# Optimization experiments

Measured on AMD Instinct MI355X. Metric: run time of the kernel, lower is better.

Reference implementation:

```python
import jax, jax.numpy as jnp
import numpy as np
import math

B, T, D, H = 4, 2048, 1024, 16
DH = D // H

def setup_inputs() -> dict:
    key = jax.random.key(0)
    ks = jax.random.split(key, 12)
    s = 1.0 / math.sqrt(D)
    inp = {
        'q': jax.random.normal(ks[0], (B, T, D), jnp.float32),
        'k': jax.random.normal(ks[1], (B, T, D), jnp.float32),
        'v': jax.random.normal(ks[2], (B, T, D), jnp.float32),
        # causal attn_mask [B, Tq, Tk]; all-keep padding mask [B,1,1,Tk]
        'attn_mask': jnp.broadcast_to(jnp.tril(jnp.ones((T, T), jnp.bool_)), (B, T, T)),
        'key_keep_mask': jnp.ones((B, 1, 1, T), jnp.bool_),
        'wq_w': jax.random.normal(ks[3], (D, D), jnp.float32) * s,
        'wq_b': jnp.zeros((D,), jnp.float32),
        'wk_w': jax.random.normal(ks[4], (D, D), jnp.float32) * s,
        'wk_b': jnp.zeros((D,), jnp.float32),
        'wv_w': jax.random.normal(ks[5], (D, D), jnp.float32) * s,
        'wv_b': jnp.zeros((D,), jnp.float32),
        'wo_w': jax.random.normal(ks[6], (D, D), jnp.float32) * s,
        'wo_b': jnp.zeros((D,), jnp.float32),
    }
    return inp

def reference(q, k, v, attn_mask, key_keep_mask, wq_w, wq_b, wk_w, wk_b, wv_w, wv_b, wo_w, wo_b):
    # projections (torch Linear: x @ W^T + b)
    Q = (q @ wq_w.T + wq_b).reshape(B, -1, H, DH).transpose(0, 2, 1, 3)  # [B,H,Tq,DH]
    K = (k @ wk_w.T + wk_b).reshape(B, -1, H, DH).transpose(0, 2, 1, 3)
    V = (v @ wv_w.T + wv_b).reshape(B, -1, H, DH).transpose(0, 2, 1, 3)
    scores = jnp.einsum('bhqd,bhkd->bhqk', Q, K) / math.sqrt(DH)
    neg_inf = jnp.array(-jnp.inf, scores.dtype)
    scores = jnp.where(attn_mask[:, None, :, :], scores, neg_inf)
    scores = jnp.where(key_keep_mask, scores, neg_inf)
    attn = jax.nn.softmax(scores, axis=-1)  # dropout p=0 -> identity
    out = jnp.einsum('bhqk,bhkd->bhqd', attn, V)
    out = out.transpose(0, 2, 1, 3).reshape(B, -1, D)
    return out @ wo_w.T + wo_b
```

## Files before the change

### kernel.cpp

```cpp
#include <hip/hip_runtime.h>
#include <cstdint>
#include <cstddef>


typedef float f32x4 __attribute__((ext_vector_type(4)));
typedef short bf16x8 __attribute__((ext_vector_type(8)));
typedef float fltx4 __attribute__((ext_vector_type(4)));
typedef unsigned short u16x4 __attribute__((ext_vector_type(4)));

#define GLOBAL_AS __attribute__((address_space(1)))
#define LDS_AS __attribute__((address_space(3)))

__device__ __forceinline__ unsigned short f2bf(float f) {
    union { float f; unsigned int u; } x;
    x.f = f;
    unsigned int u = x.u;
    unsigned int r = (u + 0x7FFFu + ((u >> 16) & 1u)) >> 16;
    return (unsigned short)r;
}

__device__ __forceinline__ unsigned int pack_trunc(float a, float b) {
    union { float f; unsigned int u; } x, y;
    x.f = a; y.f = b;
    return (x.u >> 16) | (y.u & 0xFFFF0000u);
}

__global__ __launch_bounds__(256) void cast_all_kernel(
    const float* __restrict__ q, const float* __restrict__ k, const float* __restrict__ v,
    const float* __restrict__ wq, const float* __restrict__ wk,
    const float* __restrict__ wv, const float* __restrict__ wo,
    unsigned short* __restrict__ dst)
{
    const size_t SEG = 8388608;
    const size_t WSEG = 1048576;
    size_t i = ((size_t)blockIdx.x * 256 + threadIdx.x) * 4;
    const float* src;
    size_t off;
    if (i < SEG)               { src = q;  off = i; }
    else if (i < 2 * SEG)      { src = k;  off = i - SEG; }
    else if (i < 3 * SEG)      { src = v;  off = i - 2 * SEG; }
    else if (i < 3 * SEG + WSEG)     { src = wq; off = i - 3 * SEG; }
    else if (i < 3 * SEG + 2 * WSEG) { src = wk; off = i - 3 * SEG - WSEG; }
    else if (i < 3 * SEG + 3 * WSEG) { src = wv; off = i - 3 * SEG - 2 * WSEG; }
    else                             { src = wo; off = i - 3 * SEG - 3 * WSEG; }
    fltx4 val = *(const fltx4*)(src + off);
    u16x4 o;
    o[0] = f2bf(val[0]);
    o[1] = f2bf(val[1]);
    o[2] = f2bf(val[2]);
    o[3] = f2bf(val[3]);
    *(u16x4*)(dst + i) = o;
}

__global__ __launch_bounds__(512, 2) void qkv_gemm_kernel(
    const unsigned short* __restrict__ X,
    const unsigned short* __restrict__ Wc,
    const float* __restrict__ bq, const float* __restrict__ bk,
    const float* __restrict__ bv,
    unsigned short* __restrict__ Outs,
    float qscale)
{
    const int z = blockIdx.y;
    const unsigned short* A  = X  + (size_t)z * 8388608;
    const unsigned short* Bw = Wc + (size_t)z * 1048576;
    const float* bias = (z == 0) ? bq : (z == 1) ? bk : bv;
    unsigned short* outp = Outs + (size_t)z * 8388608;
    const float scale = (z == 0) ? qscale : 1.0f;
    const bool vmode = (z == 2);

    __shared__ __align__(16) unsigned short lds[3 * 24576];

    const int tid = threadIdx.x;
    const int w = tid >> 6, lane = tid & 63;
    const int quad = lane >> 4, l16 = lane & 15;
    const int wr = w >> 1, wc = w & 1;

    const int lin = blockIdx.x;
    const int r_ = lin & 7, s_ = lin >> 3;
    const int bm = (r_ * 4 + (s_ & 3)) * 256;
    const int bn = (s_ >> 2) * 128;

    const int rsub = lane >> 3;
    const int csw = (lane & 7) ^ rsub;

    auto stage_half = [&](int kt, int buf, int half) {
        unsigned short* lA = lds + buf * 24576;
        unsigned short* lB = lA + 16384;
        const unsigned short* Ab = A + (size_t)bm * 1024 + kt * 64;
        const unsigned short* Bb = Bw + (size_t)bn * 1024 + kt * 64;
#pragma unroll
        for (int j = 0; j < 2; ++j) {
            int r0 = w * 32 + (half * 2 + j) * 8;
            __builtin_amdgcn_global_load_lds(
                (const GLOBAL_AS unsigned int*)(Ab + (size_t)(r0 + rsub) * 1024 + csw * 8),
                (LDS_AS unsigned int*)(lA + r0 * 64), 16, 0, 0);
        }
        {
            int r0 = w * 16 + half * 8;
            __builtin_amdgcn_global_load_lds(
                (const GLOBAL_AS unsigned int*)(Bb + (size_t)(r0 + rsub) * 1024 + csw * 8),
                (LDS_AS unsigned int*)(lB + r0 * 64), 16, 0, 0);
        }
    };

    f32x4 acc[4][4] = {};

    stage_half(0, 0, 0); stage_half(0, 0, 1);
    stage_half(1, 1, 0); stage_half(1, 1, 1);
    asm volatile("s_waitcnt vmcnt(6)" ::: "memory");
    __builtin_amdgcn_s_barrier();

    for (int kt = 0; kt < 16; ++kt) {
        const int cur = kt % 3;
        const int nxt = (kt + 2) % 3;
        const bool pre = (kt < 14);
        const unsigned short* lA = lds + cur * 24576;
        const unsigned short* lB = lA + 16384;

#pragma unroll
        for (int kh = 0; kh < 2; ++kh) {
            bf16x8 af[4], bfr[4];
#pragma unroll
            for (int mi = 0; mi < 4; ++mi) {
                int row = wr * 64 + mi * 16 + l16;
                af[mi] = *(const bf16x8*)(lA + (size_t)row * 64 +
                                          (((kh * 4 + quad) ^ (row & 7)) * 8));
            }
#pragma unroll
            for (int ni = 0; ni < 4; ++ni) {
                int row = wc * 64 + ni * 16 + l16;
                bfr[ni] = *(const bf16x8*)(lB + (size_t)row * 64 +
                                           (((kh * 4 + quad) ^ (row & 7)) * 8));
            }
            if (pre) stage_half(kt + 2, nxt, kh);

            __builtin_amdgcn_s_barrier();
            asm volatile("s_waitcnt lgkmcnt(0)" ::: "memory");
            __builtin_amdgcn_sched_barrier(0);
            __builtin_amdgcn_s_setprio(1);
#pragma unroll
            for (int mi = 0; mi < 4; ++mi)
#pragma unroll
                for (int ni = 0; ni < 4; ++ni)
                    acc[mi][ni] = __builtin_amdgcn_mfma_f32_16x16x32_bf16(
                        af[mi], bfr[ni], acc[mi][ni], 0, 0, 0);
            __builtin_amdgcn_s_setprio(0);
            __builtin_amdgcn_sched_barrier(0);

            if (kh == 0) {
                __builtin_amdgcn_s_barrier();
            } else {
                if (kt < 14)       asm volatile("s_waitcnt vmcnt(6)" ::: "memory");
                else if (kt == 14) asm volatile("s_waitcnt vmcnt(0)" ::: "memory");
                if (kt < 15) __builtin_amdgcn_s_barrier();
            }
        }
    }

#pragma unroll
    for (int mi = 0; mi < 4; ++mi) {
        int rowb = bm + wr * 64 + mi * 16 + quad * 4;
#pragma unroll
        for (int ni = 0; ni < 4; ++ni) {
            int col = bn + wc * 64 + ni * 16 + l16;
            float bv_ = bias[col];
#pragma unroll
            for (int r = 0; r < 4; ++r) {
                int m = rowb + r;
                float vout = (acc[mi][ni][r] + bv_) * scale;
                int b = m >> 11, t = m & 2047, h = col >> 6, d = col & 63;
                if (!vmode) {
                    outp[((size_t)(b * 16 + h) * 2048 + t) * 64 + d] = f2bf(vout);
                } else {
                    outp[((size_t)(b * 16 + h) * 64 + d) * 2048 + t] = f2bf(vout);
                }
            }
        }
    }
}

__global__ __launch_bounds__(512, 2) void out_gemm_kernel(
    const unsigned short* __restrict__ A,
    const unsigned short* __restrict__ Bw,
    const float* __restrict__ bias,
    float* __restrict__ outp)
{
    __shared__ __align__(16) unsigned short lds[3 * 24576];

    const int tid = threadIdx.x;
    const int w = tid >> 6, lane = tid & 63;
    const int quad = lane >> 4, l16 = lane & 15;
    const int wr = w >> 1, wc = w & 1;

    const int lin = blockIdx.x;
    const int r_ = lin & 7, s_ = lin >> 3;
    const int bm = (r_ * 4 + (s_ & 3)) * 256;
    const int bn = (s_ >> 2) * 128;

    const int rsub = lane >> 3;
    const int csw = (lane & 7) ^ rsub;

    auto stage_half = [&](int kt, int buf, int half) {
        unsigned short* lA = lds + buf * 24576;
        unsigned short* lB = lA + 16384;
        const unsigned short* Ab = A + (size_t)bm * 1024 + kt * 64;
        const unsigned short* Bb = Bw + (size_t)bn * 1024 + kt * 64;
#pragma unroll
        for (int j = 0; j < 2; ++j) {
            int r0 = w * 32 + (half * 2 + j) * 8;
            __builtin_amdgcn_global_load_lds(
                (const GLOBAL_AS unsigned int*)(Ab + (size_t)(r0 + rsub) * 1024 + csw * 8),
                (LDS_AS unsigned int*)(lA + r0 * 64), 16, 0, 0);
        }
        {
            int r0 = w * 16 + half * 8;
            __builtin_amdgcn_global_load_lds(
                (const GLOBAL_AS unsigned int*)(Bb + (size_t)(r0 + rsub) * 1024 + csw * 8),
                (LDS_AS unsigned int*)(lB + r0 * 64), 16, 0, 0);
        }
    };

    f32x4 acc[4][4] = {};

    stage_half(0, 0, 0); stage_half(0, 0, 1);
    stage_half(1, 1, 0); stage_half(1, 1, 1);
    asm volatile("s_waitcnt vmcnt(6)" ::: "memory");
    __builtin_amdgcn_s_barrier();

    for (int kt = 0; kt < 16; ++kt) {
        const int cur = kt % 3;
        const int nxt = (kt + 2) % 3;
        const bool pre = (kt < 14);
        const unsigned short* lA = lds + cur * 24576;
        const unsigned short* lB = lA + 16384;

#pragma unroll
        for (int kh = 0; kh < 2; ++kh) {
            bf16x8 af[4], bfr[4];
#pragma unroll
            for (int mi = 0; mi < 4; ++mi) {
                int row = wr * 64 + mi * 16 + l16;
                af[mi] = *(const bf16x8*)(lA + (size_t)row * 64 +
                                          (((kh * 4 + quad) ^ (row & 7)) * 8));
            }
#pragma unroll
            for (int ni = 0; ni < 4; ++ni) {
                int row = wc * 64 + ni * 16 + l16;
                bfr[ni] = *(const bf16x8*)(lB + (size_t)row * 64 +
                                           (((kh * 4 + quad) ^ (row & 7)) * 8));
            }
            if (pre) stage_half(kt + 2, nxt, kh);

            __builtin_amdgcn_s_barrier();
            asm volatile("s_waitcnt lgkmcnt(0)" ::: "memory");
            __builtin_amdgcn_sched_barrier(0);
            __builtin_amdgcn_s_setprio(1);
#pragma unroll
            for (int mi = 0; mi < 4; ++mi)
#pragma unroll
                for (int ni = 0; ni < 4; ++ni)
                    acc[mi][ni] = __builtin_amdgcn_mfma_f32_16x16x32_bf16(
                        af[mi], bfr[ni], acc[mi][ni], 0, 0, 0);
            __builtin_amdgcn_s_setprio(0);
            __builtin_amdgcn_sched_barrier(0);

            if (kh == 0) {
                __builtin_amdgcn_s_barrier();
            } else {
                if (kt < 14)       asm volatile("s_waitcnt vmcnt(6)" ::: "memory");
                else if (kt == 14) asm volatile("s_waitcnt vmcnt(0)" ::: "memory");
                if (kt < 15) __builtin_amdgcn_s_barrier();
            }
        }
    }

#pragma unroll
    for (int mi = 0; mi < 4; ++mi) {
        int rowb = bm + wr * 64 + mi * 16 + quad * 4;
#pragma unroll
        for (int ni = 0; ni < 4; ++ni) {
            int col = bn + wc * 64 + ni * 16 + l16;
            float bv_ = bias[col];
#pragma unroll
            for (int r = 0; r < 4; ++r)
                outp[(size_t)(rowb + r) * 1024 + col] = acc[mi][ni][r] + bv_;
        }
    }
}

__global__ __launch_bounds__(256) void attn_kernel(
    const unsigned short* __restrict__ Qh,
    const unsigned short* __restrict__ Kh,
    const unsigned short* __restrict__ Vt,
    unsigned short* __restrict__ att)
{
    const int tid = threadIdx.x;
    const int w = tid >> 6, lane = tid & 63;
    const int qd = lane >> 4, l16 = lane & 15;
    const int bh = blockIdx.x;
    const int pairy = blockIdx.y;

    const unsigned short* Qp = Qh + (size_t)bh * 2048 * 64;
    const unsigned short* Kp = Kh + (size_t)bh * 2048 * 64;
    const unsigned short* Vp = Vt + (size_t)bh * 64 * 2048;
    const int b = bh >> 4, h = bh & 15;

    __shared__ __align__(16) unsigned short Kl[3][64 * 64];
    __shared__ __align__(16) unsigned short Vl[3][64 * 64];
    __shared__ __align__(16) unsigned short Pl[4][2][16 * 64];

    auto stage = [&](int kt, int buf) {
#pragma unroll
        for (int j = 0; j < 2; ++j) {
            int r = w * 16 + j * 8 + (lane >> 3);
            int c = (lane & 7) ^ (r & 7);
            __builtin_amdgcn_global_load_lds(
                (const GLOBAL_AS unsigned int*)(Kp + (size_t)(kt * 64 + r) * 64 + c * 8),
                (LDS_AS unsigned int*)(&Kl[buf][(w * 16 + j * 8) * 64]), 16, 0, 0);
            __builtin_amdgcn_global_load_lds(
                (const GLOBAL_AS unsigned int*)(Vp + (size_t)r * 2048 + kt * 64 + c * 8),
                (LDS_AS unsigned int*)(&Vl[buf][(w * 16 + j * 8) * 64]), 16, 0, 0);
        }
    };

    auto run_phase = [&](int qblk) {
        const int wqbase = qblk * 128 + w * 32;
        const int ktmax = 2 * qblk + 1;

        bf16x8 qa[2][2];
#pragma unroll
        for (int qt = 0; qt < 2; ++qt)
#pragma unroll
            for (int ks = 0; ks < 2; ++ks)
                qa[qt][ks] = *(const bf16x8*)(Qp + (size_t)(wqbase + qt * 16 + l16) * 64 + ks * 32 + qd * 8);

        float lp[2] = {0.0f, 0.0f};
        f32x4 O[2][4] = {};

        __builtin_amdgcn_s_barrier();
        stage(0, 0);
        stage(1, 1);

        for (int kt = 0; kt <= ktmax; ++kt) {
            if (kt < ktmax) asm volatile("s_waitcnt vmcnt(4)" ::: "memory");
            else            asm volatile("s_waitcnt vmcnt(0)" ::: "memory");
            __builtin_amdgcn_s_barrier();
            if (kt + 2 <= ktmax) stage(kt + 2, (kt + 2) % 3);

            if (kt * 64 <= wqbase + 31) {
                const unsigned short* kl = &Kl[kt % 3][0];
                const unsigned short* vl = &Vl[kt % 3][0];

                bf16x8 kf[4][2];
#pragma unroll
                for (int nt = 0; nt < 4; ++nt)
#pragma unroll
                    for (int ks = 0; ks < 2; ++ks)
                        kf[nt][ks] = *(const bf16x8*)(kl + (nt * 16 + l16) * 64 +
                                                      (((ks * 4 + qd) ^ (l16 & 7)) * 8));

                f32x4 S[2][4];
                __builtin_amdgcn_s_setprio(1);
#pragma unroll
                for (int qt = 0; qt < 2; ++qt)
#pragma unroll
                    for (int nt = 0; nt < 4; ++nt) {
                        f32x4 a = {};
                        a = __builtin_amdgcn_mfma_f32_16x16x32_bf16(kf[nt][0], qa[qt][0], a, 0, 0, 0);
                        a = __builtin_amdgcn_mfma_f32_16x16x32_bf16(kf[nt][1], qa[qt][1], a, 0, 0, 0);
                        S[qt][nt] = a;
                    }
                __builtin_amdgcn_s_setprio(0);

                bf16x8 vf[2][4];
#pragma unroll
                for (int s = 0; s < 2; ++s)
#pragma unroll
                    for (int dh = 0; dh < 4; ++dh)
                        vf[s][dh] = *(const bf16x8*)(vl + (dh * 16 + l16) * 64 +
                                                     (((s * 4 + qd) ^ (l16 & 7)) * 8));

                if (kt * 64 + 63 > wqbase) {
#pragma unroll
                    for (int qt = 0; qt < 2; ++qt) {
                        int qrow = wqbase + qt * 16 + l16;
#pragma unroll
                        for (int nt = 0; nt < 4; ++nt) {
                            int kbase = kt * 64 + nt * 16 + qd * 4;
#pragma unroll
                            for (int r = 0; r < 4; ++r)
                                if (kbase + r > qrow) S[qt][nt][r] = -INFINITY;
                        }
                    }
                }

#pragma unroll
                for (int qt = 0; qt < 2; ++qt) {
                    float s0 = 0.0f;
#pragma unroll
                    for (int nt = 0; nt < 4; ++nt)
#pragma unroll
                        for (int r = 0; r < 4; ++r) {
                            float e = __builtin_amdgcn_exp2f(S[qt][nt][r]);
                            S[qt][nt][r] = e;
                            s0 += e;
                        }
                    lp[qt] += s0;
                }

#pragma unroll
                for (int qt = 0; qt < 2; ++qt) {
                    unsigned short* pw = &Pl[w][qt][0];
#pragma unroll
                    for (int nt = 0; nt < 4; ++nt) {
                        uint2 pv;
                        pv.x = pack_trunc(S[qt][nt][0], S[qt][nt][1]);
                        pv.y = pack_trunc(S[qt][nt][2], S[qt][nt][3]);
                        int chunk = (2 * nt + (qd >> 1)) ^ (l16 & 7);
                        *(uint2*)(pw + l16 * 64 + chunk * 8 + (qd & 1) * 4) = pv;
                    }
                }
                asm volatile("s_waitcnt lgkmcnt(0)" ::: "memory");

                bf16x8 pa[2][2];
#pragma unroll
                for (int qt = 0; qt < 2; ++qt)
#pragma unroll
                    for (int s = 0; s < 2; ++s)
                        pa[qt][s] = *(const bf16x8*)(&Pl[w][qt][0] + l16 * 64 +
                                                     (((s * 4 + qd) ^ (l16 & 7)) * 8));

                __builtin_amdgcn_s_setprio(1);
#pragma unroll
                for (int qt = 0; qt < 2; ++qt)
#pragma unroll
                    for (int dh = 0; dh < 4; ++dh) {
                        O[qt][dh] = __builtin_amdgcn_mfma_f32_16x16x32_bf16(pa[qt][0], vf[0][dh], O[qt][dh], 0, 0, 0);
                        O[qt][dh] = __builtin_amdgcn_mfma_f32_16x16x32_bf16(pa[qt][1], vf[1][dh], O[qt][dh], 0, 0, 0);
                    }
                __builtin_amdgcn_s_setprio(0);
            }
        }

#pragma unroll
        for (int qt = 0; qt < 2; ++qt) {
            float lsum = lp[qt];
            lsum += __shfl_xor(lsum, 16, 64);
            lsum += __shfl_xor(lsum, 32, 64);
            float linv = 1.0f / lsum;
#pragma unroll
            for (int r = 0; r < 4; ++r) {
                float lC = __shfl(linv, qd * 4 + r, 64);
                int t = wqbase + qt * 16 + qd * 4 + r;
#pragma unroll
                for (int dh = 0; dh < 4; ++dh) {
                    size_t idx = (size_t)(b * 2048 + t) * 1024 + h * 64 + dh * 16 + l16;
                    att[idx] = f2bf(O[qt][dh][r] * lC);
                }
            }
        }
    };

    run_phase(15 - pairy);
    run_phase(pairy);
}

extern "C" void kernel_launch(void* const* d_in, const int* in_sizes, int n_in,
                              void* d_out, int out_size, void* d_ws, size_t ws_size,
                              hipStream_t stream)
{
    const float* q = (const float*)d_in[0];
    const float* k = (const float*)d_in[1];
    const float* v = (const float*)d_in[2];
    const float* wq_w = (const float*)d_in[5];
    const float* wq_b = (const float*)d_in[6];
    const float* wk_w = (const float*)d_in[7];
    const float* wk_b = (const float*)d_in[8];
    const float* wv_w = (const float*)d_in[9];
    const float* wv_b = (const float*)d_in[10];
    const float* wo_w = (const float*)d_in[11];
    const float* wo_b = (const float*)d_in[12];

    unsigned short* ws = (unsigned short*)d_ws;
    unsigned short* xq  = ws;
    unsigned short* wqc = ws + 25165824;
    unsigned short* woc = ws + 28311552;
    unsigned short* Qhp = ws + 29360128;
    unsigned short* Khp = ws + 37748736;
    unsigned short* Vtp = ws + 46137344;
    unsigned short* att = xq;

    (void)in_sizes; (void)n_in; (void)out_size; (void)ws_size;

    cast_all_kernel<<<28672, 256, 0, stream>>>(q, k, v, wq_w, wk_w, wv_w, wo_w, ws);

    qkv_gemm_kernel<<<dim3(256, 3), 512, 0, stream>>>(
        xq, wqc, wq_b, wk_b, wv_b, Qhp, 0.1803368801f);

    attn_kernel<<<dim3(64, 8), 256, 0, stream>>>(Qhp, Khp, Vtp, att);

    out_gemm_kernel<<<dim3(256), 512, 0, stream>>>(att, woc, wo_b, (float*)d_out);
}
```

Before: 350.2 us.

## Retile output GEMM to 128x128 blocks with 256 threads and BK=32 pipeline

Rewrites the output projection GEMM to use 128x128 tiles with 4 waves (256 threads) and a K-step of 32 over a triple-buffered global-to-LDS pipeline, launching 512 blocks instead of 256. The LDS swizzle and wait/barrier schedule are redone for the narrower K tile, with one barrier per step instead of several. The aim is higher occupancy and better CU fill for a GEMM that is only a small part of the total time. In exchange it adds more barriers per unit of work and loses some operand reuse compared with the 256x128 tile.

```diff
diff --git a/kernel.cpp b/kernel.cpp
--- a/kernel.cpp
+++ b/kernel.cpp
@@ -179,13 +179,13 @@
     }
 }
 
-__global__ __launch_bounds__(512, 2) void out_gemm_kernel(
+__global__ __launch_bounds__(256, 3) void out_gemm_kernel(
     const unsigned short* __restrict__ A,
     const unsigned short* __restrict__ Bw,
     const float* __restrict__ bias,
     float* __restrict__ outp)
 {
-    __shared__ __align__(16) unsigned short lds[3 * 24576];
+    __shared__ __align__(16) unsigned short lds[3 * 8192];
 
     const int tid = threadIdx.x;
     const int w = tid >> 6, lane = tid & 63;
@@ -194,84 +194,64 @@
 
     const int lin = blockIdx.x;
     const int r_ = lin & 7, s_ = lin >> 3;
-    const int bm = (r_ * 4 + (s_ & 3)) * 256;
-    const int bn = (s_ >> 2) * 128;
-
-    const int rsub = lane >> 3;
-    const int csw = (lane & 7) ^ rsub;
-
-    auto stage_half = [&](int kt, int buf, int half) {
-        unsigned short* lA = lds + buf * 24576;
-        unsigned short* lB = lA + 16384;
-        const unsigned short* Ab = A + (size_t)bm * 1024 + kt * 64;
-        const unsigned short* Bb = Bw + (size_t)bn * 1024 + kt * 64;
-#pragma unroll
-        for (int j = 0; j < 2; ++j) {
-            int r0 = w * 32 + (half * 2 + j) * 8;
-            __builtin_amdgcn_global_load_lds(
-                (const GLOBAL_AS unsigned int*)(Ab + (size_t)(r0 + rsub) * 1024 + csw * 8),
-                (LDS_AS unsigned int*)(lA + r0 * 64), 16, 0, 0);
-        }
-        {
-            int r0 = w * 16 + half * 8;
-            __builtin_amdgcn_global_load_lds(
-                (const GLOBAL_AS unsigned int*)(Bb + (size_t)(r0 + rsub) * 1024 + csw * 8),
-                (LDS_AS unsigned int*)(lB + r0 * 64), 16, 0, 0);
+    const int bm = ((r_ << 3) | (s_ & 7)) * 128;
+    const int bn = (s_ >> 3) * 128;
+
+    const int rq = lane >> 2;
+    const int cq = lane & 3;
+
+    auto stage = [&](int kt, int buf) {
+        unsigned short* lA = lds + buf * 8192;
+        unsigned short* lB = lA + 4096;
+#pragma unroll
+        for (int g = 0; g < 2; ++g) {
+            int r0 = w * 32 + g * 16;
+            int row = r0 + rq;
+            int csw = cq ^ ((row >> 1) & 3);
+            __builtin_amdgcn_global_load_lds(
+                (const GLOBAL_AS unsigned int*)(A + (size_t)(bm + row) * 1024 + kt * 32 + csw * 8),
+                (LDS_AS unsigned int*)(lA + r0 * 32), 16, 0, 0);
+            __builtin_amdgcn_global_load_lds(
+                (const GLOBAL_AS unsigned int*)(Bw + (size_t)(bn + row) * 1024 + kt * 32 + csw * 8),
+                (LDS_AS unsigned int*)(lB + r0 * 32), 16, 0, 0);
         }
     };
 
     f32x4 acc[4][4] = {};
 
-    stage_half(0, 0, 0); stage_half(0, 0, 1);
-    stage_half(1, 1, 0); stage_half(1, 1, 1);
-    asm volatile("s_waitcnt vmcnt(6)" ::: "memory");
-    __builtin_amdgcn_s_barrier();
-
-    for (int kt = 0; kt < 16; ++kt) {
+    stage(0, 0);
+    stage(1, 1);
+
+    for (int kt = 0; kt < 32; ++kt) {
         const int cur = kt % 3;
-        const int nxt = (kt + 2) % 3;
-        const bool pre = (kt < 14);
-        const unsigned short* lA = lds + cur * 24576;
-        const unsigned short* lB = lA + 16384;
-
-#pragma unroll
-        for (int kh = 0; kh < 2; ++kh) {
-            bf16x8 af[4], bfr[4];
-#pragma unroll
-            for (int mi = 0; mi < 4; ++mi) {
-                int row = wr * 64 + mi * 16 + l16;
-                af[mi] = *(const bf16x8*)(lA + (size_t)row * 64 +
-                                          (((kh * 4 + quad) ^ (row & 7)) * 8));
-            }
-#pragma unroll
-            for (int ni = 0; ni < 4; ++ni) {
-                int row = wc * 64 + ni * 16 + l16;
-                bfr[ni] = *(const bf16x8*)(lB + (size_t)row * 64 +
-                                           (((kh * 4 + quad) ^ (row & 7)) * 8));
-            }
-            if (pre) stage_half(kt + 2, nxt, kh);
-
-            __builtin_amdgcn_s_barrier();
-            asm volatile("s_waitcnt lgkmcnt(0)" ::: "memory");
-            __builtin_amdgcn_sched_barrier(0);
-            __builtin_amdgcn_s_setprio(1);
-#pragma unroll
-            for (int mi = 0; mi < 4; ++mi)
-#pragma unroll
-                for (int ni = 0; ni < 4; ++ni)
-                    acc[mi][ni] = __builtin_amdgcn_mfma_f32_16x16x32_bf16(
-                        af[mi], bfr[ni], acc[mi][ni], 0, 0, 0);
-            __builtin_amdgcn_s_setprio(0);
-            __builtin_amdgcn_sched_barrier(0);
-
-            if (kh == 0) {
-                __builtin_amdgcn_s_barrier();
-            } else {
-                if (kt < 14)       asm volatile("s_waitcnt vmcnt(6)" ::: "memory");
-                else if (kt == 14) asm volatile("s_waitcnt vmcnt(0)" ::: "memory");
-                if (kt < 15) __builtin_amdgcn_s_barrier();
-            }
-        }
+        if (kt < 31) asm volatile("s_waitcnt vmcnt(4)" ::: "memory");
+        else         asm volatile("s_waitcnt vmcnt(0)" ::: "memory");
+        __builtin_amdgcn_sched_barrier(0);
+        __builtin_amdgcn_s_barrier();
+        __builtin_amdgcn_sched_barrier(0);
+        if (kt < 30) stage(kt + 2, (kt + 2) % 3);
+
+        const unsigned short* lA = lds + cur * 8192;
+        const unsigned short* lB = lA + 4096;
+        bf16x8 af[4], bfr[4];
+#pragma unroll
+        for (int mi = 0; mi < 4; ++mi) {
+            int row = wr * 64 + mi * 16 + l16;
+            af[mi] = *(const bf16x8*)(lA + row * 32 + ((quad ^ ((row >> 1) & 3)) * 8));
+        }
+#pragma unroll
+        for (int ni = 0; ni < 4; ++ni) {
+            int row = wc * 64 + ni * 16 + l16;
+            bfr[ni] = *(const bf16x8*)(lB + row * 32 + ((quad ^ ((row >> 1) & 3)) * 8));
+        }
+        __builtin_amdgcn_s_setprio(1);
+#pragma unroll
+        for (int mi = 0; mi < 4; ++mi)
+#pragma unroll
+            for (int ni = 0; ni < 4; ++ni)
+                acc[mi][ni] = __builtin_amdgcn_mfma_f32_16x16x32_bf16(
+                    af[mi], bfr[ni], acc[mi][ni], 0, 0, 0);
+        __builtin_amdgcn_s_setprio(0);
     }
 
 #pragma unroll
@@ -499,5 +479,5 @@
 
     attn_kernel<<<dim3(64, 8), 256, 0, stream>>>(Qhp, Khp, Vtp, att);
 
-    out_gemm_kernel<<<dim3(256), 512, 0, stream>>>(att, woc, wo_b, (float*)d_out);
-}
+    out_gemm_kernel<<<512, 256, 0, stream>>>(att, woc, wo_b, (float*)d_out);
+}
```

Result: no change. 349.1 us (-0.3%).
